# Performance work log

Hardware: AMD Instinct MI355X
Metric: run time of the kernel (lower is better)

Reference implementation:

```python
import jax, jax.numpy as jnp
import numpy as np

T = 4096
INPUT_SIZE = 64
DIMS = 64          # __init__ forces dimensions = input_size
RESERVOIR = 2048
OUTPUT_SIZE = 1
SPECTRAL_RADIUS = 0.95


def setup_inputs() -> dict:
    key = jax.random.key(0)
    k_x, k_c, k_in, k_res, k_w, k_b = jax.random.split(key, 6)
    X = jax.random.normal(k_x, (T, INPUT_SIZE, 1), dtype=jnp.float32)
    # conversion matrix: random then QR -> orthonormal columns
    C_raw = jax.random.uniform(k_c, (DIMS, INPUT_SIZE), dtype=jnp.float32)
    C, _ = jnp.linalg.qr(C_raw)
    # ESN weights. W_res entries ~ N(0, 1/RESERVOIR): circular-law spectral
    # radius ~= 1, scaled to the target spectral radius.
    W_in = jax.random.uniform(k_in, (RESERVOIR, DIMS), dtype=jnp.float32, minval=-1.0, maxval=1.0)
    W_res = jax.random.normal(k_res, (RESERVOIR, RESERVOIR), dtype=jnp.float32) * (SPECTRAL_RADIUS / np.sqrt(RESERVOIR))
    dense_W = jax.random.normal(k_w, (OUTPUT_SIZE, RESERVOIR + DIMS), dtype=jnp.float32) * 0.02
    dense_b = jnp.zeros((OUTPUT_SIZE,), dtype=jnp.float32)
    return {"X": X, "C": C, "W_in": W_in, "W_res": W_res,
            "dense_W": dense_W, "dense_b": dense_b}


def reference(X, C, W_in, W_res, dense_W, dense_b):
    # project all inputs up front: u_t = C @ x_t   -> (T, DIMS)
    U = jnp.einsum('di,tio->tdo', C, X)[..., 0]
    # sequential reservoir recurrence: h_t = tanh(W_in u_t + W_res h_{t-1})
    def step(h, u):
        h_new = jnp.tanh(W_in @ u + W_res @ h)
        return h_new, h_new
    h0 = jnp.zeros((W_res.shape[0],), dtype=X.dtype)
    _, H = jax.lax.scan(step, h0, U)            # (T, RESERVOIR)
    # ESN forward returns vstack(u, h); dense1 reads its transpose
    feats = jnp.concatenate([U, H], axis=1)     # (T, DIMS + RESERVOIR)
    y = feats @ dense_W.T + dense_b             # (T, OUTPUT_SIZE)
    # torch: stack of (1, OUTPUT) rows -> (T,1,OUT), permute(0,2,1) -> (T,OUT,1)
    return y[:, :, None]
```

## Files before the change

### kernel.cpp

```cpp
#include <hip/hip_runtime.h>

#define TT 4096

typedef __attribute__((ext_vector_type(2))) unsigned int u2v;
typedef __attribute__((ext_vector_type(4))) unsigned int u4v;
typedef __attribute__((ext_vector_type(2))) __fp16 f16x2;
typedef __attribute__((ext_vector_type(2))) _Float16 F16x2;
union HU { unsigned int u; f16x2 hf; F16x2 hF; };


__global__ void esn_prep(const float* __restrict__ C,
                         const float* __restrict__ Win,
                         const float* __restrict__ dW,
                         float* __restrict__ M,
                         float* __restrict__ wtil) {
  __shared__ float s[64];
  const int b = blockIdx.x, i = threadIdx.x;
  if (b < 2048) {
    s[i] = Win[b * 64 + i];
    __syncthreads();
    float acc = 0.f;
#pragma unroll 16
    for (int d = 0; d < 64; ++d) acc += s[d] * C[d * 64 + i];
    M[b * 64 + i] = acc;
  } else {
    s[i] = dW[i];
    __syncthreads();
    float acc = 0.f;
    for (int d = 0; d < 64; ++d) acc += s[d] * C[d * 64 + i];
    wtil[i] = acc;
  }
}

__device__ __forceinline__ float fast_tanh(float x) {
  const float e = __builtin_amdgcn_exp2f(x * 2.8853900817779268f);
  return 1.0f - 2.0f * __builtin_amdgcn_rcpf(e + 1.0f);
}

__device__ __forceinline__ float fdot2f(const HU a, const HU b, float c) {
#if __has_builtin(__builtin_amdgcn_fdot2)
  return __builtin_amdgcn_fdot2(a.hF, b.hF, c, false);
#else
  return c + (float)a.hf.x * (float)b.hf.x + (float)a.hf.y * (float)b.hf.y;
#endif
}

__global__ __launch_bounds__(1024) void esn_recur(
    const float* __restrict__ X, const float* __restrict__ M,
    const float* __restrict__ W, const float* __restrict__ dW,
    unsigned int* __restrict__ hpub, float* __restrict__ yp) {
  __shared__ unsigned int shh[1024];
  __shared__ unsigned int pub[16];
  __shared__ float psm[16];
  const int tid = threadIdx.x;
  const int lane = tid & 63;
  const int wave = tid >> 6;
  const int b = blockIdx.x;
  const int half = lane >> 5;
  const int li = lane & 31;
  const int r0 = b * 32 + wave * 2;
  const int row = r0 + half;
  const float ma = M[row * 64 + li];
  const float mb = M[row * 64 + li + 32];
  const float dw0 = dW[64 + r0];
  const float dw1 = dW[64 + r0 + 1];
  u4v w[8];
#pragma unroll
  for (int m = 0; m < 8; ++m) {
    const float* p = W + (size_t)row * 2048 + 256 * m + 8 * li;
    const float4 a = *(const float4*)p;
    const float4 c = *(const float4*)(p + 4);
    HU t0, t1, t2, t3;
    t0.hf = __builtin_amdgcn_cvt_pkrtz(a.x, a.y);
    t1.hf = __builtin_amdgcn_cvt_pkrtz(a.z, a.w);
    t2.hf = __builtin_amdgcn_cvt_pkrtz(c.x, c.y);
    t3.hf = __builtin_amdgcn_cvt_pkrtz(c.z, c.w);
    w[m][0] = t0.u; w[m][1] = t1.u; w[m][2] = t2.u; w[m][3] = t3.u;
  }
  shh[tid] = 0u;
  __syncthreads();

  float xa = X[li];
  float xb = X[li + 32];

  for (int t = 0; t < TT; ++t) {
    float acc = ma * xa + mb * xb;
#pragma unroll
    for (int m = 0; m < 8; ++m) {
      const u4v hv = *(const u4v*)(shh + 4 * li + 128 * m);
#pragma unroll
      for (int k = 0; k < 4; ++k) {
        HU ha, wv;
        ha.u = hv[k]; wv.u = w[m][k];
        acc = fdot2f(wv, ha, acc);
      }
    }
#pragma unroll
    for (int off = 16; off; off >>= 1) acc += __shfl_xor(acc, off, 64);
    const float other = __shfl_xor(acc, 32, 64);
    if (lane == 0) {
      const float h0 = fast_tanh(acc);
      const float h1 = fast_tanh(other);
      HU pk; pk.hf = __builtin_amdgcn_cvt_pkrtz(h0, h1);
      pub[wave] = pk.u;
      psm[wave] = dw0 * h0 + dw1 * h1;
    }
    __syncthreads();
    const unsigned tg = (unsigned)t + 1u;
    unsigned int* slot = hpub + ((t & 1) << 11);
    const int tn = (t + 1 < TT) ? t + 1 : t;
    const float xan = X[tn * 64 + li];
    const float xbn = X[tn * 64 + li + 32];
    if (wave == 1) {
      if (t + 1 < TT && lane < 16) {
        u2v pv; pv.x = pub[lane]; pv.y = tg;
        asm volatile("global_store_dwordx2 %0, %1, off sc0 sc1"
                     :: "v"(slot + 2 * (16 * b + lane)), "v"(pv) : "memory");
      }
    } else if (wave == 0) {
      if (t + 1 < TT) {
        const unsigned int* b0 = slot + 2 * lane;
        const unsigned int* b1 = b0 + 1024;
        u2v q0, q1, q2, q3, q4, q5, q6, q7, q8, q9, qa, qb, qc, qd, qe, qf;
        for (;;) {
          asm volatile(
              "global_load_dwordx2 %0, %16, off sc0 sc1\n\t"
              "global_load_dwordx2 %1, %16, off offset:512 sc0 sc1\n\t"
              "global_load_dwordx2 %2, %16, off offset:1024 sc0 sc1\n\t"
              "global_load_dwordx2 %3, %16, off offset:1536 sc0 sc1\n\t"
              "global_load_dwordx2 %4, %16, off offset:2048 sc0 sc1\n\t"
              "global_load_dwordx2 %5, %16, off offset:2560 sc0 sc1\n\t"
              "global_load_dwordx2 %6, %16, off offset:3072 sc0 sc1\n\t"
              "global_load_dwordx2 %7, %16, off offset:3584 sc0 sc1\n\t"
              "global_load_dwordx2 %8, %17, off sc0 sc1\n\t"
              "global_load_dwordx2 %9, %17, off offset:512 sc0 sc1\n\t"
              "global_load_dwordx2 %10, %17, off offset:1024 sc0 sc1\n\t"
              "global_load_dwordx2 %11, %17, off offset:1536 sc0 sc1\n\t"
              "global_load_dwordx2 %12, %17, off offset:2048 sc0 sc1\n\t"
              "global_load_dwordx2 %13, %17, off offset:2560 sc0 sc1\n\t"
              "global_load_dwordx2 %14, %17, off offset:3072 sc0 sc1\n\t"
              "global_load_dwordx2 %15, %17, off offset:3584 sc0 sc1\n\t"
              "s_waitcnt vmcnt(0)"
              : "=&v"(q0), "=&v"(q1), "=&v"(q2), "=&v"(q3),
                "=&v"(q4), "=&v"(q5), "=&v"(q6), "=&v"(q7),
                "=&v"(q8), "=&v"(q9), "=&v"(qa), "=&v"(qb),
                "=&v"(qc), "=&v"(qd), "=&v"(qe), "=&v"(qf)
              : "v"(b0), "v"(b1)
              : "memory");
          bool ok = (q0.y == tg) && (q1.y == tg) && (q2.y == tg) &&
                    (q3.y == tg) && (q4.y == tg) && (q5.y == tg) &&
                    (q6.y == tg) && (q7.y == tg) && (q8.y == tg) &&
                    (q9.y == tg) && (qa.y == tg) && (qb.y == tg) &&
                    (qc.y == tg) && (qd.y == tg) && (qe.y == tg) &&
                    (qf.y == tg);
          if (__all(ok)) break;
        }
        shh[lane] = q0.x;          shh[64 + lane] = q1.x;
        shh[128 + lane] = q2.x;    shh[192 + lane] = q3.x;
        shh[256 + lane] = q4.x;    shh[320 + lane] = q5.x;
        shh[384 + lane] = q6.x;    shh[448 + lane] = q7.x;
        shh[512 + lane] = q8.x;    shh[576 + lane] = q9.x;
        shh[640 + lane] = qa.x;    shh[704 + lane] = qb.x;
        shh[768 + lane] = qc.x;    shh[832 + lane] = qd.x;
        shh[896 + lane] = qe.x;    shh[960 + lane] = qf.x;
      }
    } else if (tid == 128) {
      float s = 0.f;
#pragma unroll
      for (int wv = 0; wv < 16; ++wv) s += psm[wv];
      yp[t * 64 + b] = s;
    }
    __syncthreads();
    xa = xan;
    xb = xbn;
  }
}

__global__ void esn_out(const float* __restrict__ X,
                        const float* __restrict__ wtil,
                        const float* __restrict__ yp,
                        const float* __restrict__ bptr,
                        float* __restrict__ out) {
  const int tid = threadIdx.x;
  const int lane = tid & 63;
  const int wave = tid >> 6;
  const int t = blockIdx.x * 4 + wave;
  float v = wtil[lane] * X[t * 64 + lane] + yp[t * 64 + lane];
#pragma unroll
  for (int off = 32; off; off >>= 1) v += __shfl_xor(v, off, 64);
  if (lane == 0) out[t] = v + bptr[0];
}

extern "C" void kernel_launch(void* const* d_in, const int* in_sizes, int n_in,
                              void* d_out, int out_size, void* d_ws, size_t ws_size,
                              hipStream_t stream) {
  const float* X   = (const float*)d_in[0];
  const float* C   = (const float*)d_in[1];
  const float* Win = (const float*)d_in[2];
  const float* W   = (const float*)d_in[3];
  const float* dW  = (const float*)d_in[4];
  const float* db  = (const float*)d_in[5];
  float* ws   = (float*)d_ws;
  float* M    = ws;
  float* wtil = ws + 131072;
  float* yp   = ws + 131200;
  unsigned int* hpub = (unsigned int*)(ws + 393344);

  esn_prep<<<2049, 64, 0, stream>>>(C, Win, dW, M, wtil);

  void* args[] = {(void*)&X, (void*)&M, (void*)&W, (void*)&dW,
                  (void*)&hpub, (void*)&yp};
  (void)hipLaunchCooperativeKernel(reinterpret_cast<void*>(&esn_recur), dim3(64),
                                   dim3(1024), args, 0, stream);

  esn_out<<<1024, 256, 0, stream>>>(X, wtil, yp, db, (float*)d_out);
}
```

Baseline: 8.757 ms.

## Split recurrence block into dedicated compute waves and communication waves

The 1024-thread block is now split into roles. Waves 8-15 each compute four reservoir rows, with 16 lanes per row holding twice as many fp16 weights in registers. Waves 0-7 only publish the new hidden state, poll the global flags and write the dense partial. Both groups meet at two barriers per step. This keeps the compute waves' register load away from the polling code, but each compute wave now does twice the dot-product work serially, and the per-step X loads are no longer prefetched.

Result: no change. 8.751 ms, median of 2 (-0.1%).

```diff
diff --git a/kernel.cpp b/kernel.cpp
--- a/kernel.cpp
+++ b/kernel.cpp
@@ -51,128 +51,139 @@
     unsigned int* __restrict__ hpub, float* __restrict__ yp) {
   __shared__ unsigned int shh[1024];
   __shared__ unsigned int pub[16];
-  __shared__ float psm[16];
+  __shared__ float psm[8];
   const int tid = threadIdx.x;
   const int lane = tid & 63;
   const int wave = tid >> 6;
   const int b = blockIdx.x;
-  const int half = lane >> 5;
-  const int li = lane & 31;
-  const int r0 = b * 32 + wave * 2;
-  const int row = r0 + half;
-  const float ma = M[row * 64 + li];
-  const float mb = M[row * 64 + li + 32];
-  const float dw0 = dW[64 + r0];
-  const float dw1 = dW[64 + r0 + 1];
-  u4v w[8];
-#pragma unroll
-  for (int m = 0; m < 8; ++m) {
-    const float* p = W + (size_t)row * 2048 + 256 * m + 8 * li;
-    const float4 a = *(const float4*)p;
-    const float4 c = *(const float4*)(p + 4);
-    HU t0, t1, t2, t3;
-    t0.hf = __builtin_amdgcn_cvt_pkrtz(a.x, a.y);
-    t1.hf = __builtin_amdgcn_cvt_pkrtz(a.z, a.w);
-    t2.hf = __builtin_amdgcn_cvt_pkrtz(c.x, c.y);
-    t3.hf = __builtin_amdgcn_cvt_pkrtz(c.z, c.w);
-    w[m][0] = t0.u; w[m][1] = t1.u; w[m][2] = t2.u; w[m][3] = t3.u;
-  }
   shh[tid] = 0u;
   __syncthreads();
 
-  float xa = X[li];
-  float xb = X[li + 32];
-
-  for (int t = 0; t < TT; ++t) {
-    float acc = ma * xa + mb * xb;
-#pragma unroll
-    for (int m = 0; m < 8; ++m) {
-      const u4v hv = *(const u4v*)(shh + 4 * li + 128 * m);
-#pragma unroll
-      for (int k = 0; k < 4; ++k) {
-        HU ha, wv;
-        ha.u = hv[k]; wv.u = w[m][k];
-        acc = fdot2f(wv, ha, acc);
+  if (wave >= 8) {
+    const int cw = wave - 8;
+    const int q = lane >> 4;
+    const int ql = lane & 15;
+    const int row = b * 32 + cw * 4 + q;
+    float m[4], dwv[4];
+#pragma unroll
+    for (int j = 0; j < 4; ++j) m[j] = M[row * 64 + ql + 16 * j];
+#pragma unroll
+    for (int r = 0; r < 4; ++r) dwv[r] = dW[64 + b * 32 + cw * 4 + r];
+    u4v w[16];
+#pragma unroll
+    for (int mm = 0; mm < 16; ++mm) {
+      const float* p = W + (size_t)row * 2048 + 128 * mm + 8 * ql;
+      const float4 a = *(const float4*)p;
+      const float4 c = *(const float4*)(p + 4);
+      HU t0, t1, t2, t3;
+      t0.hf = __builtin_amdgcn_cvt_pkrtz(a.x, a.y);
+      t1.hf = __builtin_amdgcn_cvt_pkrtz(a.z, a.w);
+      t2.hf = __builtin_amdgcn_cvt_pkrtz(c.x, c.y);
+      t3.hf = __builtin_amdgcn_cvt_pkrtz(c.z, c.w);
+      w[mm][0] = t0.u; w[mm][1] = t1.u; w[mm][2] = t2.u; w[mm][3] = t3.u;
+    }
+    for (int t = 0; t < TT; ++t) {
+      float xr[4];
+#pragma unroll
+      for (int j = 0; j < 4; ++j) xr[j] = X[t * 64 + ql + 16 * j];
+      float acc = 0.f;
+#pragma unroll
+      for (int mm = 0; mm < 16; ++mm) {
+        const u4v hv = *(const u4v*)(shh + 4 * ql + 64 * mm);
+#pragma unroll
+        for (int k = 0; k < 4; ++k) {
+          HU ha, wv;
+          ha.u = hv[k]; wv.u = w[mm][k];
+          acc = fdot2f(wv, ha, acc);
+        }
       }
+      acc += m[0] * xr[0] + m[1] * xr[1] + m[2] * xr[2] + m[3] * xr[3];
+#pragma unroll
+      for (int off = 8; off; off >>= 1) acc += __shfl_xor(acc, off, 64);
+      const float s1 = __shfl(acc, 16, 64);
+      const float s2 = __shfl(acc, 32, 64);
+      const float s3 = __shfl(acc, 48, 64);
+      if (lane == 0) {
+        const float h0 = fast_tanh(acc);
+        const float h1 = fast_tanh(s1);
+        const float h2 = fast_tanh(s2);
+        const float h3 = fast_tanh(s3);
+        HU pa, pb;
+        pa.hf = __builtin_amdgcn_cvt_pkrtz(h0, h1);
+        pb.hf = __builtin_amdgcn_cvt_pkrtz(h2, h3);
+        pub[2 * cw] = pa.u;
+        pub[2 * cw + 1] = pb.u;
+        psm[cw] = dwv[0] * h0 + dwv[1] * h1 + dwv[2] * h2 + dwv[3] * h3;
+      }
+      __syncthreads();
+      __syncthreads();
     }
-#pragma unroll
-    for (int off = 16; off; off >>= 1) acc += __shfl_xor(acc, off, 64);
-    const float other = __shfl_xor(acc, 32, 64);
-    if (lane == 0) {
-      const float h0 = fast_tanh(acc);
-      const float h1 = fast_tanh(other);
-      HU pk; pk.hf = __builtin_amdgcn_cvt_pkrtz(h0, h1);
-      pub[wave] = pk.u;
-      psm[wave] = dw0 * h0 + dw1 * h1;
+  } else {
+    for (int t = 0; t < TT; ++t) {
+      __syncthreads();
+      const unsigned tg = (unsigned)t + 1u;
+      unsigned int* slot = hpub + ((t & 1) << 11);
+      if (wave == 1) {
+        if (t + 1 < TT && lane < 16) {
+          u2v pv; pv.x = pub[lane]; pv.y = tg;
+          asm volatile("global_store_dwordx2 %0, %1, off sc0 sc1"
+                       :: "v"(slot + 2 * (16 * b + lane)), "v"(pv) : "memory");
+        }
+      } else if (wave == 0) {
+        if (t + 1 < TT) {
+          const unsigned int* b0 = slot + 2 * lane;
+          const unsigned int* b1 = b0 + 1024;
+          u2v q0, q1, q2, q3, q4, q5, q6, q7, q8, q9, qa, qb, qc, qd, qe, qf;
+          for (;;) {
+            asm volatile(
+                "global_load_dwordx2 %0, %16, off sc0 sc1\n\t"
+                "global_load_dwordx2 %1, %16, off offset:512 sc0 sc1\n\t"
+                "global_load_dwordx2 %2, %16, off offset:1024 sc0 sc1\n\t"
+                "global_load_dwordx2 %3, %16, off offset:1536 sc0 sc1\n\t"
+                "global_load_dwordx2 %4, %16, off offset:2048 sc0 sc1\n\t"
+                "global_load_dwordx2 %5, %16, off offset:2560 sc0 sc1\n\t"
+                "global_load_dwordx2 %6, %16, off offset:3072 sc0 sc1\n\t"
+                "global_load_dwordx2 %7, %16, off offset:3584 sc0 sc1\n\t"
+                "global_load_dwordx2 %8, %17, off sc0 sc1\n\t"
+                "global_load_dwordx2 %9, %17, off offset:512 sc0 sc1\n\t"
+                "global_load_dwordx2 %10, %17, off offset:1024 sc0 sc1\n\t"
+                "global_load_dwordx2 %11, %17, off offset:1536 sc0 sc1\n\t"
+                "global_load_dwordx2 %12, %17, off offset:2048 sc0 sc1\n\t"
+                "global_load_dwordx2 %13, %17, off offset:2560 sc0 sc1\n\t"
+                "global_load_dwordx2 %14, %17, off offset:3072 sc0 sc1\n\t"
+                "global_load_dwordx2 %15, %17, off offset:3584 sc0 sc1\n\t"
+                "s_waitcnt vmcnt(0)"
+                : "=&v"(q0), "=&v"(q1), "=&v"(q2), "=&v"(q3),
+                  "=&v"(q4), "=&v"(q5), "=&v"(q6), "=&v"(q7),
+                  "=&v"(q8), "=&v"(q9), "=&v"(qa), "=&v"(qb),
+                  "=&v"(qc), "=&v"(qd), "=&v"(qe), "=&v"(qf)
+                : "v"(b0), "v"(b1)
+                : "memory");
+            bool ok = (q0.y == tg) && (q1.y == tg) && (q2.y == tg) &&
+                      (q3.y == tg) && (q4.y == tg) && (q5.y == tg) &&
+                      (q6.y == tg) && (q7.y == tg) && (q8.y == tg) &&
+                      (q9.y == tg) && (qa.y == tg) && (qb.y == tg) &&
+                      (qc.y == tg) && (qd.y == tg) && (qe.y == tg) &&
+                      (qf.y == tg);
+            if (__all(ok)) break;
+          }
+          shh[lane] = q0.x;          shh[64 + lane] = q1.x;
+          shh[128 + lane] = q2.x;    shh[192 + lane] = q3.x;
+          shh[256 + lane] = q4.x;    shh[320 + lane] = q5.x;
+          shh[384 + lane] = q6.x;    shh[448 + lane] = q7.x;
+          shh[512 + lane] = q8.x;    shh[576 + lane] = q9.x;
+          shh[640 + lane] = qa.x;    shh[704 + lane] = qb.x;
+          shh[768 + lane] = qc.x;    shh[832 + lane] = qd.x;
+          shh[896 + lane] = qe.x;    shh[960 + lane] = qf.x;
+        }
+      } else if (tid == 128) {
+        float s = 0.f;
+#pragma unroll
+        for (int wv = 0; wv < 8; ++wv) s += psm[wv];
+        yp[t * 64 + b] = s;
+      }
+      __syncthreads();
     }
-    __syncthreads();
-    const unsigned tg = (unsigned)t + 1u;
-    unsigned int* slot = hpub + ((t & 1) << 11);
-    const int tn = (t + 1 < TT) ? t + 1 : t;
-    const float xan = X[tn * 64 + li];
-    const float xbn = X[tn * 64 + li + 32];
-    if (wave == 1) {
-      if (t + 1 < TT && lane < 16) {
-        u2v pv; pv.x = pub[lane]; pv.y = tg;
-        asm volatile("global_store_dwordx2 %0, %1, off sc0 sc1"
-                     :: "v"(slot + 2 * (16 * b + lane)), "v"(pv) : "memory");
-      }
-    } else if (wave == 0) {
-      if (t + 1 < TT) {
-        const unsigned int* b0 = slot + 2 * lane;
-        const unsigned int* b1 = b0 + 1024;
-        u2v q0, q1, q2, q3, q4, q5, q6, q7, q8, q9, qa, qb, qc, qd, qe, qf;
-        for (;;) {
-          asm volatile(
-              "global_load_dwordx2 %0, %16, off sc0 sc1\n\t"
-              "global_load_dwordx2 %1, %16, off offset:512 sc0 sc1\n\t"
-              "global_load_dwordx2 %2, %16, off offset:1024 sc0 sc1\n\t"
-              "global_load_dwordx2 %3, %16, off offset:1536 sc0 sc1\n\t"
-              "global_load_dwordx2 %4, %16, off offset:2048 sc0 sc1\n\t"
-              "global_load_dwordx2 %5, %16, off offset:2560 sc0 sc1\n\t"
-              "global_load_dwordx2 %6, %16, off offset:3072 sc0 sc1\n\t"
-              "global_load_dwordx2 %7, %16, off offset:3584 sc0 sc1\n\t"
-              "global_load_dwordx2 %8, %17, off sc0 sc1\n\t"
-              "global_load_dwordx2 %9, %17, off offset:512 sc0 sc1\n\t"
-              "global_load_dwordx2 %10, %17, off offset:1024 sc0 sc1\n\t"
-              "global_load_dwordx2 %11, %17, off offset:1536 sc0 sc1\n\t"
-              "global_load_dwordx2 %12, %17, off offset:2048 sc0 sc1\n\t"
-              "global_load_dwordx2 %13, %17, off offset:2560 sc0 sc1\n\t"
-              "global_load_dwordx2 %14, %17, off offset:3072 sc0 sc1\n\t"
-              "global_load_dwordx2 %15, %17, off offset:3584 sc0 sc1\n\t"
-              "s_waitcnt vmcnt(0)"
-              : "=&v"(q0), "=&v"(q1), "=&v"(q2), "=&v"(q3),
-                "=&v"(q4), "=&v"(q5), "=&v"(q6), "=&v"(q7),
-                "=&v"(q8), "=&v"(q9), "=&v"(qa), "=&v"(qb),
-                "=&v"(qc), "=&v"(qd), "=&v"(qe), "=&v"(qf)
-              : "v"(b0), "v"(b1)
-              : "memory");
-          bool ok = (q0.y == tg) && (q1.y == tg) && (q2.y == tg) &&
-                    (q3.y == tg) && (q4.y == tg) && (q5.y == tg) &&
-                    (q6.y == tg) && (q7.y == tg) && (q8.y == tg) &&
-                    (q9.y == tg) && (qa.y == tg) && (qb.y == tg) &&
-                    (qc.y == tg) && (qd.y == tg) && (qe.y == tg) &&
-                    (qf.y == tg);
-          if (__all(ok)) break;
-        }
-        shh[lane] = q0.x;          shh[64 + lane] = q1.x;
-        shh[128 + lane] = q2.x;    shh[192 + lane] = q3.x;
-        shh[256 + lane] = q4.x;    shh[320 + lane] = q5.x;
-        shh[384 + lane] = q6.x;    shh[448 + lane] = q7.x;
-        shh[512 + lane] = q8.x;    shh[576 + lane] = q9.x;
-        shh[640 + lane] = qa.x;    shh[704 + lane] = qb.x;
-        shh[768 + lane] = qc.x;    shh[832 + lane] = qd.x;
-        shh[896 + lane] = qe.x;    shh[960 + lane] = qf.x;
-      }
-    } else if (tid == 128) {
-      float s = 0.f;
-#pragma unroll
-      for (int wv = 0; wv < 16; ++wv) s += psm[wv];
-      yp[t * 64 + b] = s;
-    }
-    __syncthreads();
-    xa = xan;
-    xb = xbn;
   }
 }
 
```
